# Kernel optimization log

Hardware: AMD Instinct MI355X
Metric: run time of the kernel (lower is better)

## Reference

```python
import jax, jax.numpy as jnp
import numpy as np

E = 512
H = 8
D = E // H
EPS = 1e-5


def _ln(x, g, b):
    m = jnp.mean(x, axis=-1, keepdims=True)
    v = jnp.mean((x - m) ** 2, axis=-1, keepdims=True)
    return (x - m) * jax.lax.rsqrt(v + EPS) * g + b


def _mha_seq1(q_in, kv_in, in_w, in_b, out_w, out_b):
    # q_in, kv_in: (B, E); seq_len == 1 for both query and key/value.
    wq, wk, wv = in_w[:E], in_w[E:2 * E], in_w[2 * E:]
    bq, bk, bv = in_b[:E], in_b[E:2 * E], in_b[2 * E:]
    q = q_in @ wq.T + bq
    k = kv_in @ wk.T + bk
    v = kv_in @ wv.T + bv
    B = q.shape[0]
    qh = q.reshape(B, H, D)
    kh = k.reshape(B, H, D)
    vh = v.reshape(B, H, D)
    # scores over kv axis of length 1 -> softmax yields exactly 1
    scores = jnp.sum(qh * kh, axis=-1, keepdims=True) / np.sqrt(D).astype(np.float32)  # (B,H,1)
    w = jax.nn.softmax(scores, axis=-1)  # all ones, kept for faithfulness
    attn = (w * vh).reshape(B, E)
    return attn @ out_w.T + out_b


def _ffn(x, w1, b1, w2, b2):
    return jax.nn.relu(x @ w1.T + b1) @ w2.T + b2


def setup_inputs() -> dict:
    key = jax.random.key(0)
    ks = jax.random.split(key, 16)
    s = 0.02
    return {
        "dna": jax.random.normal(ks[0], (32768, E), jnp.float32),
        "mol": jax.random.normal(ks[1], (32768, E), jnp.float32),
        "a1_in_w": jax.random.normal(ks[2], (3 * E, E), jnp.float32) * s,
        "a1_in_b": jnp.zeros((3 * E,), jnp.float32),
        "a1_out_w": jax.random.normal(ks[3], (E, E), jnp.float32) * s,
        "a1_out_b": jnp.zeros((E,), jnp.float32),
        "a2_in_w": jax.random.normal(ks[4], (3 * E, E), jnp.float32) * s,
        "a2_in_b": jnp.zeros((3 * E,), jnp.float32),
        "a2_out_w": jax.random.normal(ks[5], (E, E), jnp.float32) * s,
        "a2_out_b": jnp.zeros((E,), jnp.float32),
        "ln1_g": jnp.ones((E,), jnp.float32), "ln1_b": jnp.zeros((E,), jnp.float32),
        "ln2_g": jnp.ones((E,), jnp.float32), "ln2_b": jnp.zeros((E,), jnp.float32),
        "ln3_g": jnp.ones((E,), jnp.float32), "ln3_b": jnp.zeros((E,), jnp.float32),
        "ln4_g": jnp.ones((E,), jnp.float32), "ln4_b": jnp.zeros((E,), jnp.float32),
        "f1_w1": jax.random.normal(ks[6], (2 * E, E), jnp.float32) * s,
        "f1_b1": jnp.zeros((2 * E,), jnp.float32),
        "f1_w2": jax.random.normal(ks[7], (E, 2 * E), jnp.float32) * s,
        "f1_b2": jnp.zeros((E,), jnp.float32),
        "f2_w1": jax.random.normal(ks[8], (2 * E, E), jnp.float32) * s,
        "f2_b1": jnp.zeros((2 * E,), jnp.float32),
        "f2_w2": jax.random.normal(ks[9], (E, 2 * E), jnp.float32) * s,
        "f2_b2": jnp.zeros((E,), jnp.float32),
    }


def reference(dna, mol,
              a1_in_w, a1_in_b, a1_out_w, a1_out_b,
              a2_in_w, a2_in_b, a2_out_w, a2_out_b,
              ln1_g, ln1_b, ln2_g, ln2_b, ln3_g, ln3_b, ln4_g, ln4_b,
              f1_w1, f1_b1, f1_w2, f1_b2,
              f2_w1, f2_b1, f2_w2, f2_b2):
    dna_att = _mha_seq1(dna, mol, a1_in_w, a1_in_b, a1_out_w, a1_out_b)
    dna_att = _ln(dna + dna_att, ln1_g, ln1_b)
    dna_att = _ln(dna_att + _ffn(dna_att, f1_w1, f1_b1, f1_w2, f1_b2), ln3_g, ln3_b)
    mol_att = _mha_seq1(mol, dna, a2_in_w, a2_in_b, a2_out_w, a2_out_b)
    mol_att = _ln(mol + mol_att, ln2_g, ln2_b)
    mol_att = _ln(mol_att + _ffn(mol_att, f2_w1, f2_b1, f2_w2, f2_b2), ln4_g, ln4_b)
    return jnp.concatenate([dna_att, mol_att], axis=-1)
```

## Files before the change

### kernel.cpp

```cpp
#include <hip/hip_runtime.h>
#include <stdint.h>


#define E 512
#define LNEPS 1e-5f

typedef unsigned short u16;
using u16x8   = __attribute__((ext_vector_type(8))) u16;
using shortx8 = __attribute__((ext_vector_type(8))) short;
using floatx4 = __attribute__((ext_vector_type(4))) float;

__device__ __forceinline__ float bf2f(u16 u) {
  uint32_t x = ((uint32_t)u) << 16;
  return __builtin_bit_cast(float, x);
}
__device__ __forceinline__ u16 f2bf(float f) {
  uint32_t x = __builtin_bit_cast(uint32_t, f);
  x += 0x7fffu + ((x >> 16) & 1u);
  return (u16)(x >> 16);
}

__device__ __forceinline__ void gl_lds16(const u16* g, u16* l) {
  __builtin_amdgcn_global_load_lds(
      (__attribute__((address_space(1))) uint32_t*)g,
      (__attribute__((address_space(3))) uint32_t*)l, 16, 0, 0);
}

template <bool RELU, bool OUTF32>
__global__ __launch_bounds__(256) void gemm_bt(const u16* __restrict__ A,
                                               const u16* __restrict__ W,
                                               const float* __restrict__ bias,
                                               void* __restrict__ Cout,
                                               int M, int N, int K, int ldc) {
  __shared__ u16 sbuf[3 * 12288];
  const int tid  = threadIdx.x;
  const int wave = tid >> 6;
  const int lane = tid & 63;
  const int m0 = blockIdx.y * 256;
  const int n0 = blockIdx.x * 128;
  const int wm = wave * 64;
  const int fm   = lane & 15;
  const int quad = lane >> 4;

  const floatx4 zero = {0.f, 0.f, 0.f, 0.f};
  floatx4 acc[4][8];
#pragma unroll
  for (int i = 0; i < 4; ++i)
#pragma unroll
    for (int j = 0; j < 8; ++j) acc[i][j] = zero;

  const int r4 = lane >> 2;
  const int c0 = (lane & 3) << 3;
  const u16* ApA = A + (size_t)(m0 + wave * 64 + r4) * K + c0;
  const u16* WpB = W + (size_t)(n0 + wave * 32 + r4) * K + c0;
  const size_t row16 = (size_t)16 * K;
  const int nt = K >> 5;

  auto STAGE = [&](const u16* ap, const u16* wp, int b) {
    u16* base = sbuf + b * 12288;
#pragma unroll
    for (int q = 0; q < 4; ++q)
      gl_lds16(ap + (size_t)q * row16, base + (wave * 4 + q) * 512);
#pragma unroll
    for (int q = 0; q < 2; ++q)
      gl_lds16(wp + (size_t)q * row16, base + 8192 + (wave * 2 + q) * 512);
  };
  auto COMPUTE = [&](int b) {
    const u16* bA = sbuf + b * 12288;
    const u16* bB = bA + 8192;
    shortx8 af[4];
#pragma unroll
    for (int i = 0; i < 4; ++i)
      af[i] = *(const shortx8*)(bA + (wm + i * 16 + fm) * 32 + quad * 8);
#pragma unroll
    for (int j = 0; j < 8; ++j) {
      const shortx8 bf = *(const shortx8*)(bB + (j * 16 + fm) * 32 + quad * 8);
#pragma unroll
      for (int i = 0; i < 4; ++i)
        acc[i][j] = __builtin_amdgcn_mfma_f32_16x16x32_bf16(af[i], bf, acc[i][j], 0, 0, 0);
    }
  };

  STAGE(ApA, WpB, 0);
  STAGE(ApA + 32, WpB + 32, 1);
  const u16* As = ApA + 64;
  const u16* Ws = WpB + 64;
  int sb = 2, cb = 0;

  for (int t = 0; t < nt - 1; ++t) {
    asm volatile("s_waitcnt vmcnt(6)\n\ts_barrier" ::: "memory");
    if (t < nt - 2) {
      STAGE(As, Ws, sb);
      As += 32;
      Ws += 32;
      sb = (sb == 2) ? 0 : sb + 1;
    }
    COMPUTE(cb);
    cb = (cb == 2) ? 0 : cb + 1;
  }
  asm volatile("s_waitcnt vmcnt(0)\n\ts_barrier" ::: "memory");
  COMPUTE(cb);

#pragma unroll
  for (int j = 0; j < 8; ++j) {
    const int col = n0 + j * 16 + fm;
    const float bj = bias ? bias[col] : 0.f;
#pragma unroll
    for (int i = 0; i < 4; ++i) {
      const int rb = m0 + wm + i * 16 + quad * 4;
#pragma unroll
      for (int r = 0; r < 4; ++r) {
        float v = acc[i][j][r] + bj;
        if (RELU) v = fmaxf(v, 0.f);
        if (OUTF32)
          ((float*)Cout)[(size_t)(rb + r) * ldc + col] = v;
        else
          ((u16*)Cout)[(size_t)(rb + r) * ldc + col] = f2bf(v);
      }
    }
  }
}

template <int MODE>
__global__ __launch_bounds__(256) void ln_add_kernel(const void* __restrict__ resid,
                                                     const void* __restrict__ addv,
                                                     const float* __restrict__ g,
                                                     const float* __restrict__ b,
                                                     void* __restrict__ outp, int ld) {
  const int wave = threadIdx.x >> 6;
  const int lane = threadIdx.x & 63;
  const size_t row = (size_t)blockIdx.x * 4 + wave;
  const int col = lane * 8;
  float x[8];
  if (MODE == 0) {
    const float* rp = (const float*)resid + row * E + col;
    const u16x8 a = *(const u16x8*)((const u16*)addv + row * E + col);
    const float4 r0 = *(const float4*)rp;
    const float4 r1 = *(const float4*)(rp + 4);
    x[0] = r0.x + bf2f(a[0]); x[1] = r0.y + bf2f(a[1]);
    x[2] = r0.z + bf2f(a[2]); x[3] = r0.w + bf2f(a[3]);
    x[4] = r1.x + bf2f(a[4]); x[5] = r1.y + bf2f(a[5]);
    x[6] = r1.z + bf2f(a[6]); x[7] = r1.w + bf2f(a[7]);
  } else {
    const u16x8 a = *(const u16x8*)((const u16*)resid + row * E + col);
    const float* ap = (const float*)addv + row * ld + col;
    const float4 r0 = *(const float4*)ap;
    const float4 r1 = *(const float4*)(ap + 4);
    x[0] = r0.x + bf2f(a[0]); x[1] = r0.y + bf2f(a[1]);
    x[2] = r0.z + bf2f(a[2]); x[3] = r0.w + bf2f(a[3]);
    x[4] = r1.x + bf2f(a[4]); x[5] = r1.y + bf2f(a[5]);
    x[6] = r1.z + bf2f(a[6]); x[7] = r1.w + bf2f(a[7]);
  }
  float s = 0.f, sq = 0.f;
#pragma unroll
  for (int i = 0; i < 8; ++i) {
    s += x[i];
    sq += x[i] * x[i];
  }
#pragma unroll
  for (int off = 32; off > 0; off >>= 1) {
    s += __shfl_xor(s, off);
    sq += __shfl_xor(sq, off);
  }
  const float mean = s * (1.f / E);
  const float var = sq * (1.f / E) - mean * mean;
  const float rs = rsqrtf(var + LNEPS);
  const float4 g0 = *(const float4*)(g + col);
  const float4 g1 = *(const float4*)(g + col + 4);
  const float4 b0 = *(const float4*)(b + col);
  const float4 b1 = *(const float4*)(b + col + 4);
  float y[8];
  y[0] = (x[0] - mean) * rs * g0.x + b0.x;
  y[1] = (x[1] - mean) * rs * g0.y + b0.y;
  y[2] = (x[2] - mean) * rs * g0.z + b0.z;
  y[3] = (x[3] - mean) * rs * g0.w + b0.w;
  y[4] = (x[4] - mean) * rs * g1.x + b1.x;
  y[5] = (x[5] - mean) * rs * g1.y + b1.y;
  y[6] = (x[6] - mean) * rs * g1.z + b1.z;
  y[7] = (x[7] - mean) * rs * g1.w + b1.w;
  if (MODE == 0) {
    u16x8 o;
#pragma unroll
    for (int i = 0; i < 8; ++i) o[i] = f2bf(y[i]);
    *(u16x8*)((u16*)outp + row * E + col) = o;
  } else {
    float* op = (float*)outp + row * ld + col;
    *(float4*)op = make_float4(y[0], y[1], y[2], y[3]);
    *(float4*)(op + 4) = make_float4(y[4], y[5], y[6], y[7]);
  }
}

__global__ __launch_bounds__(256) void cast_kernel(const float* __restrict__ in,
                                                   u16* __restrict__ out) {
  const size_t i = ((size_t)blockIdx.x * 256 + threadIdx.x) * 8;
  const float4 a = *(const float4*)(in + i);
  const float4 c = *(const float4*)(in + i + 4);
  u16x8 o;
  o[0] = f2bf(a.x); o[1] = f2bf(a.y); o[2] = f2bf(a.z); o[3] = f2bf(a.w);
  o[4] = f2bf(c.x); o[5] = f2bf(c.y); o[6] = f2bf(c.z); o[7] = f2bf(c.w);
  *(u16x8*)(out + i) = o;
}

__global__ __launch_bounds__(256) void transpose_cast_kernel(const float* __restrict__ in,
                                                             u16* __restrict__ out) {
  __shared__ float t[32][33];
  const int bx = blockIdx.x * 32;
  const int by = blockIdx.y * 32;
  const int x = threadIdx.x & 31;
  const int y0 = threadIdx.x >> 5;
#pragma unroll
  for (int y = y0; y < 32; y += 8) t[y][x] = in[(size_t)(by + y) * E + bx + x];
  __syncthreads();
#pragma unroll
  for (int y = y0; y < 32; y += 8) out[(size_t)(bx + y) * E + by + x] = f2bf(t[x][y]);
}

__global__ __launch_bounds__(256) void combine_bias_kernel(const float* __restrict__ outw,
                                                           const float* __restrict__ bv,
                                                           const float* __restrict__ outb,
                                                           float* __restrict__ bc) {
  const int n = blockIdx.x * 256 + threadIdx.x;
  const float* wr = outw + (size_t)n * E;
  float s = 0.f;
  for (int j = 0; j < E; j += 4) {
    const float4 w4 = *(const float4*)(wr + j);
    const float4 v4 = *(const float4*)(bv + j);
    s += w4.x * v4.x + w4.y * v4.y + w4.z * v4.z + w4.w * v4.w;
  }
  bc[n] = s + outb[n];
}

extern "C" void kernel_launch(void* const* d_in, const int* in_sizes, int n_in,
                              void* d_out, int out_size, void* d_ws, size_t ws_size,
                              hipStream_t stream) {
  const float* dna      = (const float*)d_in[0];
  const float* mol      = (const float*)d_in[1];
  const float* a1_in_w  = (const float*)d_in[2];
  const float* a1_in_b  = (const float*)d_in[3];
  const float* a1_out_w = (const float*)d_in[4];
  const float* a1_out_b = (const float*)d_in[5];
  const float* a2_in_w  = (const float*)d_in[6];
  const float* a2_in_b  = (const float*)d_in[7];
  const float* a2_out_w = (const float*)d_in[8];
  const float* a2_out_b = (const float*)d_in[9];
  const float* ln1_g = (const float*)d_in[10];
  const float* ln1_b = (const float*)d_in[11];
  const float* ln2_g = (const float*)d_in[12];
  const float* ln2_b = (const float*)d_in[13];
  const float* ln3_g = (const float*)d_in[14];
  const float* ln3_b = (const float*)d_in[15];
  const float* ln4_g = (const float*)d_in[16];
  const float* ln4_b = (const float*)d_in[17];
  const float* f1_w1 = (const float*)d_in[18];
  const float* f1_b1 = (const float*)d_in[19];
  const float* f1_w2 = (const float*)d_in[20];
  const float* f1_b2 = (const float*)d_in[21];
  const float* f2_w1 = (const float*)d_in[22];
  const float* f2_b1 = (const float*)d_in[23];
  const float* f2_w2 = (const float*)d_in[24];
  const float* f2_b2 = (const float*)d_in[25];

  const int M = in_sizes[0] / E;

  char* ws = (char*)d_ws;
  auto bump = [&](size_t sz) {
    char* p = ws;
    ws += (sz + 255) & ~(size_t)255;
    return p;
  };
  u16* wvT1   = (u16*)bump((size_t)E * E * 2);
  u16* wvT2   = (u16*)bump((size_t)E * E * 2);
  u16* outw1b = (u16*)bump((size_t)E * E * 2);
  u16* outw2b = (u16*)bump((size_t)E * E * 2);
  u16* Wc1    = (u16*)bump((size_t)E * E * 2);
  u16* Wc2    = (u16*)bump((size_t)E * E * 2);
  u16* fw11   = (u16*)bump((size_t)2 * E * E * 2);
  u16* fw12   = (u16*)bump((size_t)2 * E * E * 2);
  u16* fw21   = (u16*)bump((size_t)2 * E * E * 2);
  u16* fw22   = (u16*)bump((size_t)2 * E * E * 2);
  float* bc1  = (float*)bump(E * 4);
  float* bc2  = (float*)bump(E * 4);
  u16* X1 = (u16*)bump((size_t)M * E * 2);
  u16* X2 = (u16*)bump((size_t)M * E * 2);
  u16* Hb = (u16*)bump((size_t)M * 2 * E * 2);
  u16* H0 = Hb;
  u16* H1 = Hb + (size_t)M * E;
  float* out_f = (float*)d_out;

  transpose_cast_kernel<<<dim3(16, 16), 256, 0, stream>>>(a1_in_w + 2 * E * E, wvT1);
  transpose_cast_kernel<<<dim3(16, 16), 256, 0, stream>>>(a2_in_w + 2 * E * E, wvT2);
  cast_kernel<<<E * E / 2048, 256, 0, stream>>>(a1_out_w, outw1b);
  cast_kernel<<<E * E / 2048, 256, 0, stream>>>(a2_out_w, outw2b);
  cast_kernel<<<2 * E * E / 2048, 256, 0, stream>>>(f1_w1, fw11);
  cast_kernel<<<2 * E * E / 2048, 256, 0, stream>>>(f1_w2, fw12);
  cast_kernel<<<2 * E * E / 2048, 256, 0, stream>>>(f2_w1, fw21);
  cast_kernel<<<2 * E * E / 2048, 256, 0, stream>>>(f2_w2, fw22);
  combine_bias_kernel<<<2, 256, 0, stream>>>(a1_out_w, a1_in_b + 2 * E, a1_out_b, bc1);
  combine_bias_kernel<<<2, 256, 0, stream>>>(a2_out_w, a2_in_b + 2 * E, a2_out_b, bc2);
  gemm_bt<false, false><<<dim3(4, 2), 256, 0, stream>>>(outw1b, wvT1, nullptr, Wc1, E, E, E, E);
  gemm_bt<false, false><<<dim3(4, 2), 256, 0, stream>>>(outw2b, wvT2, nullptr, Wc2, E, E, E, E);

  cast_kernel<<<(int)((size_t)M * E / 2048), 256, 0, stream>>>(dna, X1);
  cast_kernel<<<(int)((size_t)M * E / 2048), 256, 0, stream>>>(mol, X2);
  gemm_bt<false, false><<<dim3(4, M / 256), 256, 0, stream>>>(X2, Wc1, bc1, H0, M, E, E, E);
  gemm_bt<false, false><<<dim3(4, M / 256), 256, 0, stream>>>(X1, Wc2, bc2, H1, M, E, E, E);
  ln_add_kernel<0><<<M / 4, 256, 0, stream>>>(dna, H0, ln1_g, ln1_b, X1, E);
  ln_add_kernel<0><<<M / 4, 256, 0, stream>>>(mol, H1, ln2_g, ln2_b, X2, E);
  gemm_bt<true, false><<<dim3(8, M / 256), 256, 0, stream>>>(X1, fw11, f1_b1, Hb, M, 2 * E, E, 2 * E);
  gemm_bt<false, true><<<dim3(4, M / 256), 256, 0, stream>>>(Hb, fw12, f1_b2, out_f, M, E, 2 * E, 2 * E);
  ln_add_kernel<1><<<M / 4, 256, 0, stream>>>(X1, out_f, ln3_g, ln3_b, out_f, 2 * E);
  gemm_bt<true, false><<<dim3(8, M / 256), 256, 0, stream>>>(X2, fw21, f2_b1, Hb, M, 2 * E, E, 2 * E);
  gemm_bt<false, true><<<dim3(4, M / 256), 256, 0, stream>>>(Hb, fw22, f2_b2, out_f + E, M, E, 2 * E, 2 * E);
  ln_add_kernel<1><<<M / 4, 256, 0, stream>>>(X2, out_f + E, ln4_g, ln4_b, out_f + E, 2 * E);
}
```

Measured before the change: 747.6 us.

## Batch paired branch kernels via grid z-dimension and prioritize MFMA issue

Merges the dna and mol branch launches (casts, weight prep, GEMMs, layernorms) into single launches indexed by a grid dimension, so each launch fills the GPU with twice as many blocks and the launch count drops. The second FFN GEMM now writes bf16 to a scratch buffer instead of fp32 into the output, and the final layernorm reads bf16 for both inputs. The GEMM inner loop preloads all B fragments and raises wave priority around the MFMA block. This costs extra workspace for separate per-branch hidden buffers and some precision on the FFN output before the final layernorm.

```diff
diff --git a/kernel.cpp b/kernel.cpp
--- a/kernel.cpp
+++ b/kernel.cpp
@@ -26,13 +26,23 @@
       (__attribute__((address_space(3))) uint32_t*)l, 16, 0, 0);
 }
 
-template <bool RELU, bool OUTF32>
-__global__ __launch_bounds__(256) void gemm_bt(const u16* __restrict__ A,
-                                               const u16* __restrict__ W,
-                                               const float* __restrict__ bias,
-                                               void* __restrict__ Cout,
+template <bool RELU>
+__global__ __launch_bounds__(256) void gemm_bt(const u16* __restrict__ A0,
+                                               const u16* __restrict__ W0,
+                                               const float* __restrict__ bias0,
+                                               u16* __restrict__ C0,
+                                               const u16* __restrict__ A1,
+                                               const u16* __restrict__ W1,
+                                               const float* __restrict__ bias1,
+                                               u16* __restrict__ C1,
                                                int M, int N, int K, int ldc) {
   __shared__ u16 sbuf[3 * 12288];
+  const int zz = blockIdx.z;
+  const u16* A = zz ? A1 : A0;
+  const u16* W = zz ? W1 : W0;
+  const float* bias = zz ? bias1 : bias0;
+  u16* Cout = zz ? C1 : C0;
+
   const int tid  = threadIdx.x;
   const int wave = tid >> 6;
   const int lane = tid & 63;
@@ -68,17 +78,20 @@
   auto COMPUTE = [&](int b) {
     const u16* bA = sbuf + b * 12288;
     const u16* bB = bA + 8192;
-    shortx8 af[4];
+    shortx8 af[4], bf[8];
 #pragma unroll
     for (int i = 0; i < 4; ++i)
       af[i] = *(const shortx8*)(bA + (wm + i * 16 + fm) * 32 + quad * 8);
 #pragma unroll
-    for (int j = 0; j < 8; ++j) {
-      const shortx8 bf = *(const shortx8*)(bB + (j * 16 + fm) * 32 + quad * 8);
+    for (int j = 0; j < 8; ++j)
+      bf[j] = *(const shortx8*)(bB + (j * 16 + fm) * 32 + quad * 8);
+    __builtin_amdgcn_s_setprio(1);
+#pragma unroll
+    for (int j = 0; j < 8; ++j)
 #pragma unroll
       for (int i = 0; i < 4; ++i)
-        acc[i][j] = __builtin_amdgcn_mfma_f32_16x16x32_bf16(af[i], bf, acc[i][j], 0, 0, 0);
-    }
+        acc[i][j] = __builtin_amdgcn_mfma_f32_16x16x32_bf16(af[i], bf[j], acc[i][j], 0, 0, 0);
+    __builtin_amdgcn_s_setprio(0);
   };
 
   STAGE(ApA, WpB, 0);
@@ -112,29 +125,34 @@
       for (int r = 0; r < 4; ++r) {
         float v = acc[i][j][r] + bj;
         if (RELU) v = fmaxf(v, 0.f);
-        if (OUTF32)
-          ((float*)Cout)[(size_t)(rb + r) * ldc + col] = v;
-        else
-          ((u16*)Cout)[(size_t)(rb + r) * ldc + col] = f2bf(v);
+        Cout[(size_t)(rb + r) * ldc + col] = f2bf(v);
       }
     }
   }
 }
 
 template <int MODE>
-__global__ __launch_bounds__(256) void ln_add_kernel(const void* __restrict__ resid,
-                                                     const void* __restrict__ addv,
-                                                     const float* __restrict__ g,
-                                                     const float* __restrict__ b,
-                                                     void* __restrict__ outp, int ld) {
+__global__ __launch_bounds__(256) void ln_add_kernel(
+    const void* __restrict__ resid0, const void* __restrict__ resid1,
+    const u16* __restrict__ add0, const u16* __restrict__ add1,
+    const float* __restrict__ g0, const float* __restrict__ b0,
+    const float* __restrict__ g1, const float* __restrict__ b1,
+    void* __restrict__ out0, void* __restrict__ out1, int ld) {
+  const int ss = blockIdx.y;
+  const void* resid = ss ? resid1 : resid0;
+  const u16* addv = ss ? add1 : add0;
+  const float* g = ss ? g1 : g0;
+  const float* b = ss ? b1 : b0;
+  void* outp = ss ? out1 : out0;
+
   const int wave = threadIdx.x >> 6;
   const int lane = threadIdx.x & 63;
   const size_t row = (size_t)blockIdx.x * 4 + wave;
   const int col = lane * 8;
   float x[8];
+  const u16x8 a = *(const u16x8*)(addv + row * E + col);
   if (MODE == 0) {
     const float* rp = (const float*)resid + row * E + col;
-    const u16x8 a = *(const u16x8*)((const u16*)addv + row * E + col);
     const float4 r0 = *(const float4*)rp;
     const float4 r1 = *(const float4*)(rp + 4);
     x[0] = r0.x + bf2f(a[0]); x[1] = r0.y + bf2f(a[1]);
@@ -142,14 +160,9 @@
     x[4] = r1.x + bf2f(a[4]); x[5] = r1.y + bf2f(a[5]);
     x[6] = r1.z + bf2f(a[6]); x[7] = r1.w + bf2f(a[7]);
   } else {
-    const u16x8 a = *(const u16x8*)((const u16*)resid + row * E + col);
-    const float* ap = (const float*)addv + row * ld + col;
-    const float4 r0 = *(const float4*)ap;
-    const float4 r1 = *(const float4*)(ap + 4);
-    x[0] = r0.x + bf2f(a[0]); x[1] = r0.y + bf2f(a[1]);
-    x[2] = r0.z + bf2f(a[2]); x[3] = r0.w + bf2f(a[3]);
-    x[4] = r1.x + bf2f(a[4]); x[5] = r1.y + bf2f(a[5]);
-    x[6] = r1.z + bf2f(a[6]); x[7] = r1.w + bf2f(a[7]);
+    const u16x8 rr = *(const u16x8*)((const u16*)resid + row * E + col);
+#pragma unroll
+    for (int i = 0; i < 8; ++i) x[i] = bf2f(rr[i]) + bf2f(a[i]);
   }
   float s = 0.f, sq = 0.f;
 #pragma unroll
@@ -165,19 +178,19 @@
   const float mean = s * (1.f / E);
   const float var = sq * (1.f / E) - mean * mean;
   const float rs = rsqrtf(var + LNEPS);
-  const float4 g0 = *(const float4*)(g + col);
-  const float4 g1 = *(const float4*)(g + col + 4);
-  const float4 b0 = *(const float4*)(b + col);
-  const float4 b1 = *(const float4*)(b + col + 4);
+  const float4 g0v = *(const float4*)(g + col);
+  const float4 g1v = *(const float4*)(g + col + 4);
+  const float4 b0v = *(const float4*)(b + col);
+  const float4 b1v = *(const float4*)(b + col + 4);
   float y[8];
-  y[0] = (x[0] - mean) * rs * g0.x + b0.x;
-  y[1] = (x[1] - mean) * rs * g0.y + b0.y;
-  y[2] = (x[2] - mean) * rs * g0.z + b0.z;
-  y[3] = (x[3] - mean) * rs * g0.w + b0.w;
-  y[4] = (x[4] - mean) * rs * g1.x + b1.x;
-  y[5] = (x[5] - mean) * rs * g1.y + b1.y;
-  y[6] = (x[6] - mean) * rs * g1.z + b1.z;
-  y[7] = (x[7] - mean) * rs * g1.w + b1.w;
+  y[0] = (x[0] - mean) * rs * g0v.x + b0v.x;
+  y[1] = (x[1] - mean) * rs * g0v.y + b0v.y;
+  y[2] = (x[2] - mean) * rs * g0v.z + b0v.z;
+  y[3] = (x[3] - mean) * rs * g0v.w + b0v.w;
+  y[4] = (x[4] - mean) * rs * g1v.x + b1v.x;
+  y[5] = (x[5] - mean) * rs * g1v.y + b1v.y;
+  y[6] = (x[6] - mean) * rs * g1v.z + b1v.z;
+  y[7] = (x[7] - mean) * rs * g1v.w + b1v.w;
   if (MODE == 0) {
     u16x8 o;
 #pragma unroll
@@ -190,8 +203,12 @@
   }
 }
 
-__global__ __launch_bounds__(256) void cast_kernel(const float* __restrict__ in,
-                                                   u16* __restrict__ out) {
+__global__ __launch_bounds__(256) void cast2_kernel(const float* __restrict__ in0,
+                                                    const float* __restrict__ in1,
+                                                    u16* __restrict__ o0,
+                                                    u16* __restrict__ o1) {
+  const float* in = blockIdx.y ? in1 : in0;
+  u16* out = blockIdx.y ? o1 : o0;
   const size_t i = ((size_t)blockIdx.x * 256 + threadIdx.x) * 8;
   const float4 a = *(const float4*)(in + i);
   const float4 c = *(const float4*)(in + i + 4);
@@ -201,9 +218,42 @@
   *(u16x8*)(out + i) = o;
 }
 
-__global__ __launch_bounds__(256) void transpose_cast_kernel(const float* __restrict__ in,
-                                                             u16* __restrict__ out) {
+__global__ __launch_bounds__(256) void cast6_kernel(
+    const float* __restrict__ s0, u16* __restrict__ d0,
+    const float* __restrict__ s1, u16* __restrict__ d1,
+    const float* __restrict__ s2, u16* __restrict__ d2,
+    const float* __restrict__ s3, u16* __restrict__ d3,
+    const float* __restrict__ s4, u16* __restrict__ d4,
+    const float* __restrict__ s5, u16* __restrict__ d5) {
+  int b = blockIdx.x;
+  const float* in;
+  u16* out;
+  if (b < 256) {
+    in = (b < 128) ? s0 : s1;
+    out = (b < 128) ? d0 : d1;
+    b &= 127;
+  } else {
+    const int t = (b - 256) >> 8;
+    in = (t == 0) ? s2 : (t == 1) ? s3 : (t == 2) ? s4 : s5;
+    out = (t == 0) ? d2 : (t == 1) ? d3 : (t == 2) ? d4 : d5;
+    b = (b - 256) & 255;
+  }
+  const size_t i = ((size_t)b * 256 + threadIdx.x) * 8;
+  const float4 a = *(const float4*)(in + i);
+  const float4 c = *(const float4*)(in + i + 4);
+  u16x8 o;
+  o[0] = f2bf(a.x); o[1] = f2bf(a.y); o[2] = f2bf(a.z); o[3] = f2bf(a.w);
+  o[4] = f2bf(c.x); o[5] = f2bf(c.y); o[6] = f2bf(c.z); o[7] = f2bf(c.w);
+  *(u16x8*)(out + i) = o;
+}
+
+__global__ __launch_bounds__(256) void transpose_cast2_kernel(const float* __restrict__ in0,
+                                                              u16* __restrict__ out0,
+                                                              const float* __restrict__ in1,
+                                                              u16* __restrict__ out1) {
   __shared__ float t[32][33];
+  const float* in = blockIdx.z ? in1 : in0;
+  u16* out = blockIdx.z ? out1 : out0;
   const int bx = blockIdx.x * 32;
   const int by = blockIdx.y * 32;
   const int x = threadIdx.x & 31;
@@ -215,11 +265,17 @@
   for (int y = y0; y < 32; y += 8) out[(size_t)(bx + y) * E + by + x] = f2bf(t[x][y]);
 }
 
-__global__ __launch_bounds__(256) void combine_bias_kernel(const float* __restrict__ outw,
-                                                           const float* __restrict__ bv,
-                                                           const float* __restrict__ outb,
-                                                           float* __restrict__ bc) {
-  const int n = blockIdx.x * 256 + threadIdx.x;
+__global__ __launch_bounds__(256) void combine_bias2_kernel(
+    const float* __restrict__ outw1, const float* __restrict__ bv1,
+    const float* __restrict__ outb1, float* __restrict__ bc1,
+    const float* __restrict__ outw2, const float* __restrict__ bv2,
+    const float* __restrict__ outb2, float* __restrict__ bc2) {
+  int n = blockIdx.x * 256 + threadIdx.x;
+  const float* outw = (n < E) ? outw1 : outw2;
+  const float* bv = (n < E) ? bv1 : bv2;
+  const float* outb = (n < E) ? outb1 : outb2;
+  float* bc = (n < E) ? bc1 : bc2;
+  n &= (E - 1);
   const float* wr = outw + (size_t)n * E;
   float s = 0.f;
   for (int j = 0; j < E; j += 4) {
@@ -280,36 +336,32 @@
   u16* fw22   = (u16*)bump((size_t)2 * E * E * 2);
   float* bc1  = (float*)bump(E * 4);
   float* bc2  = (float*)bump(E * 4);
-  u16* X1 = (u16*)bump((size_t)M * E * 2);
-  u16* X2 = (u16*)bump((size_t)M * E * 2);
-  u16* Hb = (u16*)bump((size_t)M * 2 * E * 2);
-  u16* H0 = Hb;
-  u16* H1 = Hb + (size_t)M * E;
+  u16* X1  = (u16*)bump((size_t)M * E * 2);
+  u16* X2  = (u16*)bump((size_t)M * E * 2);
+  u16* Hb0 = (u16*)bump((size_t)M * 2 * E * 2);
+  u16* Hb1 = (u16*)bump((size_t)M * 2 * E * 2);
+  u16* Hc0 = (u16*)bump((size_t)M * E * 2);
+  u16* Hc1 = (u16*)bump((size_t)M * E * 2);
   float* out_f = (float*)d_out;
 
-  transpose_cast_kernel<<<dim3(16, 16), 256, 0, stream>>>(a1_in_w + 2 * E * E, wvT1);
-  transpose_cast_kernel<<<dim3(16, 16), 256, 0, stream>>>(a2_in_w + 2 * E * E, wvT2);
-  cast_kernel<<<E * E / 2048, 256, 0, stream>>>(a1_out_w, outw1b);
-  cast_kernel<<<E * E / 2048, 256, 0, stream>>>(a2_out_w, outw2b);
-  cast_kernel<<<2 * E * E / 2048, 256, 0, stream>>>(f1_w1, fw11);
-  cast_kernel<<<2 * E * E / 2048, 256, 0, stream>>>(f1_w2, fw12);
-  cast_kernel<<<2 * E * E / 2048, 256, 0, stream>>>(f2_w1, fw21);
-  cast_kernel<<<2 * E * E / 2048, 256, 0, stream>>>(f2_w2, fw22);
-  combine_bias_kernel<<<2, 256, 0, stream>>>(a1_out_w, a1_in_b + 2 * E, a1_out_b, bc1);
-  combine_bias_kernel<<<2, 256, 0, stream>>>(a2_out_w, a2_in_b + 2 * E, a2_out_b, bc2);
-  gemm_bt<false, false><<<dim3(4, 2), 256, 0, stream>>>(outw1b, wvT1, nullptr, Wc1, E, E, E, E);
-  gemm_bt<false, false><<<dim3(4, 2), 256, 0, stream>>>(outw2b, wvT2, nullptr, Wc2, E, E, E, E);
-
-  cast_kernel<<<(int)((size_t)M * E / 2048), 256, 0, stream>>>(dna, X1);
-  cast_kernel<<<(int)((size_t)M * E / 2048), 256, 0, stream>>>(mol, X2);
-  gemm_bt<false, false><<<dim3(4, M / 256), 256, 0, stream>>>(X2, Wc1, bc1, H0, M, E, E, E);
-  gemm_bt<false, false><<<dim3(4, M / 256), 256, 0, stream>>>(X1, Wc2, bc2, H1, M, E, E, E);
-  ln_add_kernel<0><<<M / 4, 256, 0, stream>>>(dna, H0, ln1_g, ln1_b, X1, E);
-  ln_add_kernel<0><<<M / 4, 256, 0, stream>>>(mol, H1, ln2_g, ln2_b, X2, E);
-  gemm_bt<true, false><<<dim3(8, M / 256), 256, 0, stream>>>(X1, fw11, f1_b1, Hb, M, 2 * E, E, 2 * E);
-  gemm_bt<false, true><<<dim3(4, M / 256), 256, 0, stream>>>(Hb, fw12, f1_b2, out_f, M, E, 2 * E, 2 * E);
-  ln_add_kernel<1><<<M / 4, 256, 0, stream>>>(X1, out_f, ln3_g, ln3_b, out_f, 2 * E);
-  gemm_bt<true, false><<<dim3(8, M / 256), 256, 0, stream>>>(X2, fw21, f2_b1, Hb, M, 2 * E, E, 2 * E);
-  gemm_bt<false, true><<<dim3(4, M / 256), 256, 0, stream>>>(Hb, fw22, f2_b2, out_f + E, M, E, 2 * E, 2 * E);
-  ln_add_kernel<1><<<M / 4, 256, 0, stream>>>(X2, out_f + E, ln4_g, ln4_b, out_f + E, 2 * E);
-}
+  transpose_cast2_kernel<<<dim3(16, 16, 2), 256, 0, stream>>>(
+      a1_in_w + 2 * E * E, wvT1, a2_in_w + 2 * E * E, wvT2);
+  cast6_kernel<<<1280, 256, 0, stream>>>(a1_out_w, outw1b, a2_out_w, outw2b,
+                                         f1_w1, fw11, f1_w2, fw12, f2_w1, fw21, f2_w2, fw22);
+  combine_bias2_kernel<<<4, 256, 0, stream>>>(a1_out_w, a1_in_b + 2 * E, a1_out_b, bc1,
+                                              a2_out_w, a2_in_b + 2 * E, a2_out_b, bc2);
+  gemm_bt<false><<<dim3(4, 2, 2), 256, 0, stream>>>(
+      outw1b, wvT1, nullptr, Wc1, outw2b, wvT2, nullptr, Wc2, E, E, E, E);
+
+  cast2_kernel<<<dim3((unsigned)((size_t)M * E / 2048), 2), 256, 0, stream>>>(dna, mol, X1, X2);
+  gemm_bt<false><<<dim3(4, M / 256, 2), 256, 0, stream>>>(
+      X2, Wc1, bc1, Hc0, X1, Wc2, bc2, Hc1, M, E, E, E);
+  ln_add_kernel<0><<<dim3(M / 4, 2), 256, 0, stream>>>(
+      dna, mol, Hc0, Hc1, ln1_g, ln1_b, ln2_g, ln2_b, X1, X2, E);
+  gemm_bt<true><<<dim3(8, M / 256, 2), 256, 0, stream>>>(
+      X1, fw11, f1_b1, Hb0, X2, fw21, f2_b1, Hb1, M, 2 * E, E, 2 * E);
+  gemm_bt<false><<<dim3(4, M / 256, 2), 256, 0, stream>>>(
+      Hb0, fw12, f1_b2, Hc0, Hb1, fw22, f2_b2, Hc1, M, E, 2 * E, E);
+  ln_add_kernel<2><<<dim3(M / 4, 2), 256, 0, stream>>>(
+      X1, X2, Hc0, Hc1, ln3_g, ln3_b, ln4_g, ln4_b, out_f, out_f + E, 2 * E);
+}
```

After: 677.1 us. 1.1x faster.
